# Performance work log

Hardware: AMD Instinct MI355X
Metric: run time of the kernel (lower is better)

## Reference

```python
import jax, jax.numpy as jnp
import numpy as np

N_NODES = 50000
N_EDGES = 800000
IN_DIM = 128
HID = 64
ZDIM = 64
N_GRAPHS = 64


def gcn_conv(x, W, b, src, dst, n):
    # PyG GCNConv: add self-loops, symmetric deg^-1/2 normalization,
    # linear transform then gather-scatter aggregation.
    h = x @ W  # [N, out]
    loops = jnp.arange(n, dtype=src.dtype)
    s = jnp.concatenate([src, loops])
    d = jnp.concatenate([dst, loops])
    deg = jnp.zeros((n,), h.dtype).at[d].add(1.0)  # includes self-loops -> >=1
    dinv = jax.lax.rsqrt(deg)
    norm = dinv[s] * dinv[d]  # [E+N]
    msg = h[s] * norm[:, None]  # gather [E+N, out]
    out = jnp.zeros_like(h).at[d].add(msg)  # scatter-add
    return out + b


def mean_pool(h, batch, num_graphs):
    sums = jax.ops.segment_sum(h, batch, num_segments=num_graphs)
    cnt = jax.ops.segment_sum(jnp.ones((h.shape[0],), h.dtype), batch,
                              num_segments=num_graphs)
    return sums / jnp.maximum(cnt, 1.0)[:, None]


def setup_inputs() -> dict:
    key = jax.random.key(0)
    ks = jax.random.split(key, 9)
    x = jax.random.normal(ks[0], (N_NODES, IN_DIM), jnp.float32)
    edge_index = jax.random.randint(ks[1], (2, N_EDGES), 0, N_NODES, jnp.int64 if jax.config.jax_enable_x64 else jnp.int32)
    batch = jnp.sort(jax.random.randint(ks[2], (N_NODES,), 0, N_GRAPHS))
    s1 = 1.0 / np.sqrt(IN_DIM)
    s2 = 1.0 / np.sqrt(HID)
    W1 = jax.random.uniform(ks[3], (IN_DIM, HID), jnp.float32, -s1, s1)
    b1 = jnp.zeros((HID,), jnp.float32)
    Wmu = jax.random.uniform(ks[4], (HID, ZDIM), jnp.float32, -s2, s2)
    bmu = jnp.zeros((ZDIM,), jnp.float32)
    Wsig = jax.random.uniform(ks[5], (HID, ZDIM), jnp.float32, -s2, s2)
    bsig = jnp.zeros((ZDIM,), jnp.float32)
    return {"x": x, "edge_index": edge_index, "batch": batch,
            "num_graphs": N_GRAPHS, "W1": W1, "b1": b1,
            "Wmu": Wmu, "bmu": bmu, "Wsig": Wsig, "bsig": bsig}


def reference(x, edge_index, batch, num_graphs, W1, b1, Wmu, bmu, Wsig, bsig):
    src, dst = edge_index[0], edge_index[1]
    n = x.shape[0]
    h = jax.nn.elu(gcn_conv(x, W1, b1, src, dst, n))
    z_mu = mean_pool(jax.nn.elu(gcn_conv(h, Wmu, bmu, src, dst, n)), batch, num_graphs)
    z_sigma = mean_pool(jax.nn.elu(gcn_conv(h, Wsig, bsig, src, dst, n)), batch, num_graphs)
    return (z_mu, z_sigma)
```

## Files before the change

### kernel.cpp

```cpp
#include <hip/hip_runtime.h>
#include <hip/hip_fp16.h>


#define IN_DIM 128
#define HID 64
#define ZDIM 64
#define N_GRAPHS 64
#define SCAN_B 1024

__device__ __forceinline__ float elu1(float x) {
    return x > 0.f ? x : expm1f(x);
}

#define ACC8(RV, MV) do { \
    const __half2* _hp = (const __half2*)&(RV); \
    float2 _f0 = __half22float2(_hp[0]); \
    float2 _f1 = __half22float2(_hp[1]); \
    float2 _f2 = __half22float2(_hp[2]); \
    float2 _f3 = __half22float2(_hp[3]); \
    acc[0] = fmaf((MV), _f0.x, acc[0]); \
    acc[1] = fmaf((MV), _f0.y, acc[1]); \
    acc[2] = fmaf((MV), _f1.x, acc[2]); \
    acc[3] = fmaf((MV), _f1.y, acc[3]); \
    acc[4] = fmaf((MV), _f2.x, acc[4]); \
    acc[5] = fmaf((MV), _f2.y, acc[5]); \
    acc[6] = fmaf((MV), _f3.x, acc[6]); \
    acc[7] = fmaf((MV), _f3.y, acc[7]); \
  } while (0)

__global__ void k_count(const int* __restrict__ dst, int* __restrict__ kc,
                        int* __restrict__ rank, int E) {
    int e = blockIdx.x * blockDim.x + threadIdx.x;
    if (e < E) rank[e] = atomicAdd(&kc[dst[e]], 1);
}

__global__ __launch_bounds__(SCAN_B) void k_scan1(const int* __restrict__ kc,
                                                  int* __restrict__ bsum, int n) {
    __shared__ int wpart[16];
    int tid = threadIdx.x, lane = tid & 63, w = tid >> 6;
    int i = blockIdx.x * SCAN_B + tid;
    int v = (i < n) ? kc[i] : 0;
#pragma unroll
    for (int d = 1; d < 64; d <<= 1) v += __shfl_xor(v, d, 64);
    if (lane == 0) wpart[w] = v;
    __syncthreads();
    if (tid < 16) {
        int t = wpart[tid];
#pragma unroll
        for (int d = 1; d < 16; d <<= 1) t += __shfl_xor(t, d, 64);
        if (tid == 0) bsum[blockIdx.x] = t;
    }
}

__global__ __launch_bounds__(SCAN_B) void k_scan3(const int* __restrict__ kc,
                                                  const int* __restrict__ bsum,
                                                  int* __restrict__ offs,
                                                  float* __restrict__ dinv,
                                                  int n, int nb) {
    __shared__ int wsum[16];
    __shared__ int sbase;
    int tid = threadIdx.x, lane = tid & 63, w = tid >> 6;
    if (tid < 64) {
        int v = (tid < nb) ? bsum[tid] : 0;
        int s = v;
#pragma unroll
        for (int d = 1; d < 64; d <<= 1) {
            int u = __shfl_up(s, d, 64);
            if (tid >= d) s += u;
        }
        if (tid == blockIdx.x) sbase = s - v;
    }
    int i = blockIdx.x * SCAN_B + tid;
    int v = (i < n) ? kc[i] : 0;
    int s = v;
#pragma unroll
    for (int d = 1; d < 64; d <<= 1) {
        int u = __shfl_up(s, d, 64);
        if (lane >= d) s += u;
    }
    if (lane == 63) wsum[w] = s;
    __syncthreads();
    if (tid < 16) {
        int t = wsum[tid];
#pragma unroll
        for (int d = 1; d < 16; d <<= 1) {
            int u = __shfl_up(t, d, 64);
            if (tid >= d) t += u;
        }
        wsum[tid] = t;
    }
    __syncthreads();
    int base = sbase + ((w == 0) ? 0 : wsum[w - 1]);
    if (i < n) {
        offs[i + 1] = base + s;
        dinv[i] = 1.0f / sqrtf(1.0f + (float)v);
        if (i == 0) offs[0] = 0;
    }
}

__global__ void k_fill(const int* __restrict__ src, const int* __restrict__ dst,
                       const int* __restrict__ rank, const int* __restrict__ offs,
                       int* __restrict__ csr, int E) {
    int e = blockIdx.x * blockDim.x + threadIdx.x;
    if (e < E) csr[offs[dst[e]] + rank[e]] = src[e];
}

__global__ __launch_bounds__(256) void k_mm1(const float* __restrict__ x,
                                             const float* __restrict__ W,
                                             const float* __restrict__ dinv,
                                             __half* __restrict__ ts1h, int n) {
    __shared__ float xs[64 * 68];
    __shared__ float ws[64 * 68];
    const int tid = threadIdx.x;
    const int m0 = blockIdx.x * 64;
    const int j = tid & 15;
    const int i = tid >> 4;

    const float4* x4 = (const float4*)x;
    const float4* W4 = (const float4*)W;

    float4 acc[4];
#pragma unroll
    for (int r = 0; r < 4; ++r) acc[r] = make_float4(0.f, 0.f, 0.f, 0.f);

    for (int kk = 0; kk < IN_DIM; kk += 64) {
        __syncthreads();
        for (int idx = tid; idx < 64 * 16; idx += 256) {
            int row = idx >> 4, c4 = idx & 15;
            float4 v = make_float4(0.f, 0.f, 0.f, 0.f);
            if (m0 + row < n) v = x4[(size_t)(m0 + row) * 32 + (kk >> 2) + c4];
            *(float4*)&xs[row * 68 + 4 * c4] = v;
            *(float4*)&ws[row * 68 + 4 * c4] = W4[(size_t)(kk + row) * 16 + c4];
        }
        __syncthreads();
#pragma unroll 1
        for (int k4 = 0; k4 < 16; ++k4) {
            float4 a[4];
#pragma unroll
            for (int r = 0; r < 4; ++r)
                a[r] = *(const float4*)&xs[(4 * i + r) * 68 + 4 * k4];
#pragma unroll
            for (int kc = 0; kc < 4; ++kc) {
                float4 bv = *(const float4*)&ws[(4 * k4 + kc) * 68 + 4 * j];
#pragma unroll
                for (int r = 0; r < 4; ++r) {
                    float av = (&a[r].x)[kc];
                    acc[r].x = fmaf(av, bv.x, acc[r].x);
                    acc[r].y = fmaf(av, bv.y, acc[r].y);
                    acc[r].z = fmaf(av, bv.z, acc[r].z);
                    acc[r].w = fmaf(av, bv.w, acc[r].w);
                }
            }
        }
    }

#pragma unroll
    for (int r = 0; r < 4; ++r) {
        int row = m0 + 4 * i + r;
        if (row < n) {
            float di = dinv[row];
            float4 tv = acc[r];
            __half2* p = (__half2*)&ts1h[(size_t)row * HID + 4 * j];
            p[0] = __floats2half2_rn(tv.x * di, tv.y * di);
            p[1] = __floats2half2_rn(tv.z * di, tv.w * di);
        }
    }
}

__global__ __launch_bounds__(256) void k_gather_hh(const int* __restrict__ off,
                                                   const int* __restrict__ csr,
                                                   const float* __restrict__ dinv,
                                                   const __half* __restrict__ ts,
                                                   const float* __restrict__ b1,
                                                   __half* __restrict__ hh, int n) {
    int node = blockIdx.x * 4 + (threadIdx.x >> 6);
    if (node >= n) return;
    int lane = threadIdx.x & 63;
    int g = lane >> 3, sub = lane & 7;
    int s0 = off[node], s1 = off[node + 1];
    float acc[8];
#pragma unroll
    for (int j = 0; j < 8; ++j) acc[j] = 0.f;

    if (s1 > s0) {
        int last = s1 - 1;
        int p0 = s0 + g, p1 = p0 + 8, p2 = p0 + 16, p3 = p0 + 24;
        int i0 = csr[p0 < s1 ? p0 : last];
        int i1 = csr[p1 < s1 ? p1 : last];
        int i2 = csr[p2 < s1 ? p2 : last];
        int i3 = csr[p3 < s1 ? p3 : last];
        float4 r0 = *(const float4*)&ts[(size_t)i0 * 64 + sub * 8];
        float4 r1 = *(const float4*)&ts[(size_t)i1 * 64 + sub * 8];
        float4 r2 = *(const float4*)&ts[(size_t)i2 * 64 + sub * 8];
        float4 r3 = *(const float4*)&ts[(size_t)i3 * 64 + sub * 8];
        float m0 = (p0 < s1) ? 1.f : 0.f;
        float m1 = (p1 < s1) ? 1.f : 0.f;
        float m2 = (p2 < s1) ? 1.f : 0.f;
        float m3 = (p3 < s1) ? 1.f : 0.f;
        ACC8(r0, m0);
        ACC8(r1, m1);
        ACC8(r2, m2);
        ACC8(r3, m3);
        for (int k = s0 + 32 + g; k < s1; k += 8) {
            int iv = csr[k];
            float4 rv = *(const float4*)&ts[(size_t)iv * 64 + sub * 8];
            ACC8(rv, 1.f);
        }
    }

#pragma unroll
    for (int j = 0; j < 8; ++j) {
        acc[j] += __shfl_xor(acc[j], 8, 64);
        acc[j] += __shfl_xor(acc[j], 16, 64);
        acc[j] += __shfl_xor(acc[j], 32, 64);
    }

    if (g == 0) {
        float4 sr = *(const float4*)&ts[(size_t)node * 64 + sub * 8];
        const __half2* sh = (const __half2*)&sr;
        float di = dinv[node];
        const float4* b4 = (const float4*)b1;
        float4 ba = b4[sub * 2], bb = b4[sub * 2 + 1];
        float2 f0 = __half22float2(sh[0]);
        float2 f1 = __half22float2(sh[1]);
        float2 f2 = __half22float2(sh[2]);
        float2 f3 = __half22float2(sh[3]);
        float e0 = elu1((acc[0] + f0.x) * di + ba.x) * di;
        float e1 = elu1((acc[1] + f0.y) * di + ba.y) * di;
        float e2 = elu1((acc[2] + f1.x) * di + ba.z) * di;
        float e3 = elu1((acc[3] + f1.y) * di + ba.w) * di;
        float e4 = elu1((acc[4] + f2.x) * di + bb.x) * di;
        float e5 = elu1((acc[5] + f2.y) * di + bb.y) * di;
        float e6 = elu1((acc[6] + f3.x) * di + bb.z) * di;
        float e7 = elu1((acc[7] + f3.y) * di + bb.w) * di;
        float4 outv;
        __half2* op = (__half2*)&outv;
        op[0] = __floats2half2_rn(e0, e1);
        op[1] = __floats2half2_rn(e2, e3);
        op[2] = __floats2half2_rn(e4, e5);
        op[3] = __floats2half2_rn(e6, e7);
        *(float4*)&hh[(size_t)node * 64 + sub * 8] = outv;
    }
}

__global__ __launch_bounds__(256) void k_gather_g(const int* __restrict__ off,
                                                  const int* __restrict__ csr,
                                                  const float* __restrict__ dinv,
                                                  const __half* __restrict__ hh,
                                                  float* __restrict__ gout, int n) {
    int node = blockIdx.x * 4 + (threadIdx.x >> 6);
    if (node >= n) return;
    int lane = threadIdx.x & 63;
    int g = lane >> 3, sub = lane & 7;
    int s0 = off[node], s1 = off[node + 1];
    float acc[8];
#pragma unroll
    for (int j = 0; j < 8; ++j) acc[j] = 0.f;

    if (s1 > s0) {
        int last = s1 - 1;
        int p0 = s0 + g, p1 = p0 + 8, p2 = p0 + 16, p3 = p0 + 24;
        int i0 = csr[p0 < s1 ? p0 : last];
        int i1 = csr[p1 < s1 ? p1 : last];
        int i2 = csr[p2 < s1 ? p2 : last];
        int i3 = csr[p3 < s1 ? p3 : last];
        float4 r0 = *(const float4*)&hh[(size_t)i0 * 64 + sub * 8];
        float4 r1 = *(const float4*)&hh[(size_t)i1 * 64 + sub * 8];
        float4 r2 = *(const float4*)&hh[(size_t)i2 * 64 + sub * 8];
        float4 r3 = *(const float4*)&hh[(size_t)i3 * 64 + sub * 8];
        float m0 = (p0 < s1) ? 1.f : 0.f;
        float m1 = (p1 < s1) ? 1.f : 0.f;
        float m2 = (p2 < s1) ? 1.f : 0.f;
        float m3 = (p3 < s1) ? 1.f : 0.f;
        ACC8(r0, m0);
        ACC8(r1, m1);
        ACC8(r2, m2);
        ACC8(r3, m3);
        for (int k = s0 + 32 + g; k < s1; k += 8) {
            int iv = csr[k];
            float4 rv = *(const float4*)&hh[(size_t)iv * 64 + sub * 8];
            ACC8(rv, 1.f);
        }
    }

#pragma unroll
    for (int j = 0; j < 8; ++j) {
        acc[j] += __shfl_xor(acc[j], 8, 64);
        acc[j] += __shfl_xor(acc[j], 16, 64);
        acc[j] += __shfl_xor(acc[j], 32, 64);
    }

    if (g == 0) {
        float4 sr = *(const float4*)&hh[(size_t)node * 64 + sub * 8];
        const __half2* sh = (const __half2*)&sr;
        float di = dinv[node];
        float2 f0 = __half22float2(sh[0]);
        float2 f1 = __half22float2(sh[1]);
        float2 f2 = __half22float2(sh[2]);
        float2 f3 = __half22float2(sh[3]);
        float o0 = (acc[0] + f0.x) * di;
        float o1 = (acc[1] + f0.y) * di;
        float o2 = (acc[2] + f1.x) * di;
        float o3 = (acc[3] + f1.y) * di;
        float o4 = (acc[4] + f2.x) * di;
        float o5 = (acc[5] + f2.y) * di;
        float o6 = (acc[6] + f3.x) * di;
        float o7 = (acc[7] + f3.y) * di;
        *(float4*)&gout[(size_t)node * 64 + sub * 8] = make_float4(o0, o1, o2, o3);
        *(float4*)&gout[(size_t)node * 64 + sub * 8 + 4] = make_float4(o4, o5, o6, o7);
    }
}

__global__ __launch_bounds__(256) void k_mm_pool(const float* __restrict__ g,
                                                 const float* __restrict__ Wmu,
                                                 const float* __restrict__ Wsig,
                                                 const float* __restrict__ bmu,
                                                 const float* __restrict__ bsig,
                                                 const int* __restrict__ batch,
                                                 float* __restrict__ sums, int n) {
    __shared__ float hs[64 * 68];
    __shared__ float wc[64 * 132];
    __shared__ int bs[64];
    const int tid = threadIdx.x;
    const int m0 = blockIdx.x * 64;
    const int j = tid & 15;
    const int i = tid >> 4;

    const float4* g4 = (const float4*)g;
    const float4* Wm4 = (const float4*)Wmu;
    const float4* Ws4 = (const float4*)Wsig;
    for (int idx = tid; idx < 64 * 16; idx += 256) {
        int row = idx >> 4, c4 = idx & 15;
        float4 v = make_float4(0.f, 0.f, 0.f, 0.f);
        if (m0 + row < n) v = g4[(size_t)(m0 + row) * 16 + c4];
        *(float4*)&hs[row * 68 + 4 * c4] = v;
        *(float4*)&wc[row * 132 + 4 * c4] = Wm4[(size_t)row * 16 + c4];
        *(float4*)&wc[row * 132 + 64 + 4 * c4] = Ws4[(size_t)row * 16 + c4];
    }
    if (tid < 64) bs[tid] = (m0 + tid < n) ? batch[m0 + tid] : -1;
    __syncthreads();

    float4 accm[4], accs[4];
#pragma unroll
    for (int r = 0; r < 4; ++r) {
        accm[r] = make_float4(0.f, 0.f, 0.f, 0.f);
        accs[r] = make_float4(0.f, 0.f, 0.f, 0.f);
    }

#pragma unroll 1
    for (int k4 = 0; k4 < 16; ++k4) {
        float4 a[4];
#pragma unroll
        for (int r = 0; r < 4; ++r)
            a[r] = *(const float4*)&hs[(4 * i + r) * 68 + 4 * k4];
#pragma unroll
        for (int kc = 0; kc < 4; ++kc) {
            float4 bm = *(const float4*)&wc[(4 * k4 + kc) * 132 + 4 * j];
            float4 bsv = *(const float4*)&wc[(4 * k4 + kc) * 132 + 64 + 4 * j];
#pragma unroll
            for (int r = 0; r < 4; ++r) {
                float av = (&a[r].x)[kc];
                accm[r].x = fmaf(av, bm.x, accm[r].x);
                accm[r].y = fmaf(av, bm.y, accm[r].y);
                accm[r].z = fmaf(av, bm.z, accm[r].z);
                accm[r].w = fmaf(av, bm.w, accm[r].w);
                accs[r].x = fmaf(av, bsv.x, accs[r].x);
                accs[r].y = fmaf(av, bsv.y, accs[r].y);
                accs[r].z = fmaf(av, bsv.z, accs[r].z);
                accs[r].w = fmaf(av, bsv.w, accs[r].w);
            }
        }
    }

    float4 bm = ((const float4*)bmu)[j];
    float4 bg = ((const float4*)bsig)[j];
    __syncthreads();

#pragma unroll
    for (int r = 0; r < 4; ++r) {
        int row = 4 * i + r;
        float4 m = accm[r], s = accs[r];
        m.x = elu1(m.x + bm.x);
        m.y = elu1(m.y + bm.y);
        m.z = elu1(m.z + bm.z);
        m.w = elu1(m.w + bm.w);
        s.x = elu1(s.x + bg.x);
        s.y = elu1(s.y + bg.y);
        s.z = elu1(s.z + bg.z);
        s.w = elu1(s.w + bg.w);
        *(float4*)&wc[row * 132 + 4 * j] = m;
        *(float4*)&wc[row * 132 + 64 + 4 * j] = s;
    }
    __syncthreads();

    int d = tid & 127, seg = tid >> 7;
    int base = (d < 64) ? d : (64 * 64 - 64 + d);
    float acc = 0.f;
    int gcur = -1;
    int r0 = seg * 32;
    for (int r = r0; r < r0 + 32; ++r) {
        int gb = bs[r];
        if (gb < 0) break;
        float v = wc[r * 132 + d];
        if (gb != gcur) {
            if (gcur >= 0) atomicAdd(&sums[base + gcur * 64], acc);
            acc = 0.f;
            gcur = gb;
        }
        acc += v;
    }
    if (gcur >= 0) atomicAdd(&sums[base + gcur * 64], acc);
}

__global__ void k_pool_final(const float* __restrict__ sums,
                             const int* __restrict__ batch,
                             float* __restrict__ out, int n) {
    int i = blockIdx.x * blockDim.x + threadIdx.x;
    if (i >= 2 * N_GRAPHS * ZDIM) return;
    int g = (i >> 6) & 63;
    int lo = 0, hi = n;
    while (lo < hi) { int m = (lo + hi) >> 1; if (batch[m] < g) lo = m + 1; else hi = m; }
    int s = lo;
    lo = s; hi = n;
    while (lo < hi) { int m = (lo + hi) >> 1; if (batch[m] < g + 1) lo = m + 1; else hi = m; }
    float c = fmaxf((float)(lo - s), 1.0f);
    out[i] = sums[i] / c;
}

extern "C" void kernel_launch(void* const* d_in, const int* in_sizes, int n_in,
                              void* d_out, int out_size, void* d_ws, size_t ws_size,
                              hipStream_t stream) {
    const float* x    = (const float*)d_in[0];
    const int*   ei   = (const int*)d_in[1];
    const int*   batch= (const int*)d_in[2];
    const float* W1   = (const float*)d_in[4];
    const float* b1   = (const float*)d_in[5];
    const float* Wmu  = (const float*)d_in[6];
    const float* bmu  = (const float*)d_in[7];
    const float* Wsig = (const float*)d_in[8];
    const float* bsig = (const float*)d_in[9];
    float* out = (float*)d_out;

    const int n = in_sizes[0] / IN_DIM;
    const int E = in_sizes[1] / 2;
    const int* src = ei;
    const int* dst = ei + E;
    const int NSB = (n + SCAN_B - 1) / SCAN_B;

    float* ws = (float*)d_ws;
    size_t off_w = 0;
    int*   kc   = (int*)(ws + off_w); off_w += 50048;
    float* sums = ws + off_w; off_w += 8192;
    float* dinv = ws + off_w; off_w += 50048;
    int*   offs = (int*)(ws + off_w); off_w += 50056;
    int*   bsum = (int*)(ws + off_w); off_w += 64;
    int*   rank = (int*)(ws + off_w); off_w += 800000;
    int*   csr  = (int*)(ws + off_w); off_w += 800000;
    off_w = (off_w + 15) & ~(size_t)15;
    const size_t BIG = (size_t)n * 64;
    __half* ts1h = (__half*)(ws + off_w); off_w += BIG / 2;
    __half* hh   = (__half*)(ws + off_w); off_w += BIG / 2;
    float*  gbuf = ws + off_w; off_w += BIG;

    const int gE  = (E + 255) / 256;
    const int gNW = (n + 3) / 4;
    const int NB  = (n + 63) / 64;

    hipMemsetAsync(kc, 0, (50048 + 8192) * sizeof(int), stream);
    k_count<<<gE, 256, 0, stream>>>(dst, kc, rank, E);
    k_scan1<<<NSB, SCAN_B, 0, stream>>>(kc, bsum, n);
    k_scan3<<<NSB, SCAN_B, 0, stream>>>(kc, bsum, offs, dinv, n, NSB);
    k_fill<<<gE, 256, 0, stream>>>(src, dst, rank, offs, csr, E);

    k_mm1<<<NB, 256, 0, stream>>>(x, W1, dinv, ts1h, n);
    k_gather_hh<<<gNW, 256, 0, stream>>>(offs, csr, dinv, ts1h, b1, hh, n);

    k_gather_g<<<gNW, 256, 0, stream>>>(offs, csr, dinv, hh, gbuf, n);

    k_mm_pool<<<NB, 256, 0, stream>>>(gbuf, Wmu, Wsig, bmu, bsig, batch, sums, n);
    k_pool_final<<<(2 * N_GRAPHS * ZDIM + 255) / 256, 256, 0, stream>>>(sums, batch, out, n);
}
```

Baseline: 238.1 us.

## Split fp16 feature buffers into two 32-column halves for gather kernels

The 64-wide fp16 node feature arrays are stored as two separate 32-column planar buffers, and each gather kernel launches twice as many blocks, each handling one half for four nodes. Each wavefront now gathers 16 neighbours in parallel with 64-byte rows instead of 8 with 128-byte rows, so there are more independent loads in flight per node. Blocks for the two halves are interleaved so both halves of a node group run close together in time. The cost is twice the CSR index reads, an extra shuffle-reduction step, and more blocks overall.

```diff
diff --git a/kernel.cpp b/kernel.cpp
--- a/kernel.cpp
+++ b/kernel.cpp
@@ -108,7 +108,8 @@
 __global__ __launch_bounds__(256) void k_mm1(const float* __restrict__ x,
                                              const float* __restrict__ W,
                                              const float* __restrict__ dinv,
-                                             __half* __restrict__ ts1h, int n) {
+                                             __half* __restrict__ tsA,
+                                             __half* __restrict__ tsB, int n) {
     __shared__ float xs[64 * 68];
     __shared__ float ws[64 * 68];
     const int tid = threadIdx.x;
@@ -160,9 +161,13 @@
         if (row < n) {
             float di = dinv[row];
             float4 tv = acc[r];
-            __half2* p = (__half2*)&ts1h[(size_t)row * HID + 4 * j];
-            p[0] = __floats2half2_rn(tv.x * di, tv.y * di);
-            p[1] = __floats2half2_rn(tv.z * di, tv.w * di);
+            __half2 h0 = __floats2half2_rn(tv.x * di, tv.y * di);
+            __half2 h1 = __floats2half2_rn(tv.z * di, tv.w * di);
+            __half2* p = (j < 8)
+                ? (__half2*)&tsA[(size_t)row * 32 + 4 * j]
+                : (__half2*)&tsB[(size_t)row * 32 + 4 * (j - 8)];
+            p[0] = h0;
+            p[1] = h1;
         }
     }
 }
@@ -170,57 +175,58 @@
 __global__ __launch_bounds__(256) void k_gather_hh(const int* __restrict__ off,
                                                    const int* __restrict__ csr,
                                                    const float* __restrict__ dinv,
-                                                   const __half* __restrict__ ts,
+                                                   const __half* __restrict__ tsA,
+                                                   const __half* __restrict__ tsB,
                                                    const float* __restrict__ b1,
-                                                   __half* __restrict__ hh, int n) {
-    int node = blockIdx.x * 4 + (threadIdx.x >> 6);
+                                                   __half* __restrict__ hhA,
+                                                   __half* __restrict__ hhB, int n) {
+    int bid = blockIdx.x;
+    int half = (bid >> 2) & 1;
+    int jb = (bid >> 3) * 4 + (bid & 3);
+    int node = jb * 4 + (threadIdx.x >> 6);
     if (node >= n) return;
+    const __half* T = half ? tsB : tsA;
+    __half* H = half ? hhB : hhA;
     int lane = threadIdx.x & 63;
-    int g = lane >> 3, sub = lane & 7;
+    int g = lane >> 2, sub = lane & 3;
     int s0 = off[node], s1 = off[node + 1];
     float acc[8];
 #pragma unroll
-    for (int j = 0; j < 8; ++j) acc[j] = 0.f;
+    for (int q = 0; q < 8; ++q) acc[q] = 0.f;
 
     if (s1 > s0) {
         int last = s1 - 1;
-        int p0 = s0 + g, p1 = p0 + 8, p2 = p0 + 16, p3 = p0 + 24;
+        int p0 = s0 + g, p1 = p0 + 16;
         int i0 = csr[p0 < s1 ? p0 : last];
         int i1 = csr[p1 < s1 ? p1 : last];
-        int i2 = csr[p2 < s1 ? p2 : last];
-        int i3 = csr[p3 < s1 ? p3 : last];
-        float4 r0 = *(const float4*)&ts[(size_t)i0 * 64 + sub * 8];
-        float4 r1 = *(const float4*)&ts[(size_t)i1 * 64 + sub * 8];
-        float4 r2 = *(const float4*)&ts[(size_t)i2 * 64 + sub * 8];
-        float4 r3 = *(const float4*)&ts[(size_t)i3 * 64 + sub * 8];
+        float4 r0 = *(const float4*)&T[(size_t)i0 * 32 + sub * 8];
+        float4 r1 = *(const float4*)&T[(size_t)i1 * 32 + sub * 8];
         float m0 = (p0 < s1) ? 1.f : 0.f;
         float m1 = (p1 < s1) ? 1.f : 0.f;
-        float m2 = (p2 < s1) ? 1.f : 0.f;
-        float m3 = (p3 < s1) ? 1.f : 0.f;
         ACC8(r0, m0);
         ACC8(r1, m1);
-        ACC8(r2, m2);
-        ACC8(r3, m3);
-        for (int k = s0 + 32 + g; k < s1; k += 8) {
+        for (int k = s0 + 32 + g; k < s1; k += 16) {
             int iv = csr[k];
-            float4 rv = *(const float4*)&ts[(size_t)iv * 64 + sub * 8];
+            float4 rv = *(const float4*)&T[(size_t)iv * 32 + sub * 8];
             ACC8(rv, 1.f);
         }
     }
 
 #pragma unroll
-    for (int j = 0; j < 8; ++j) {
-        acc[j] += __shfl_xor(acc[j], 8, 64);
-        acc[j] += __shfl_xor(acc[j], 16, 64);
-        acc[j] += __shfl_xor(acc[j], 32, 64);
+    for (int q = 0; q < 8; ++q) {
+        acc[q] += __shfl_xor(acc[q], 4, 64);
+        acc[q] += __shfl_xor(acc[q], 8, 64);
+        acc[q] += __shfl_xor(acc[q], 16, 64);
+        acc[q] += __shfl_xor(acc[q], 32, 64);
     }
 
     if (g == 0) {
-        float4 sr = *(const float4*)&ts[(size_t)node * 64 + sub * 8];
+        float4 sr = *(const float4*)&T[(size_t)node * 32 + sub * 8];
         const __half2* sh = (const __half2*)&sr;
         float di = dinv[node];
         const float4* b4 = (const float4*)b1;
-        float4 ba = b4[sub * 2], bb = b4[sub * 2 + 1];
+        float4 ba = b4[half * 8 + sub * 2];
+        float4 bb = b4[half * 8 + sub * 2 + 1];
         float2 f0 = __half22float2(sh[0]);
         float2 f1 = __half22float2(sh[1]);
         float2 f2 = __half22float2(sh[2]);
@@ -239,59 +245,57 @@
         op[1] = __floats2half2_rn(e2, e3);
         op[2] = __floats2half2_rn(e4, e5);
         op[3] = __floats2half2_rn(e6, e7);
-        *(float4*)&hh[(size_t)node * 64 + sub * 8] = outv;
+        *(float4*)&H[(size_t)node * 32 + sub * 8] = outv;
     }
 }
 
 __global__ __launch_bounds__(256) void k_gather_g(const int* __restrict__ off,
                                                   const int* __restrict__ csr,
                                                   const float* __restrict__ dinv,
-                                                  const __half* __restrict__ hh,
+                                                  const __half* __restrict__ hhA,
+                                                  const __half* __restrict__ hhB,
                                                   float* __restrict__ gout, int n) {
-    int node = blockIdx.x * 4 + (threadIdx.x >> 6);
+    int bid = blockIdx.x;
+    int half = (bid >> 2) & 1;
+    int jb = (bid >> 3) * 4 + (bid & 3);
+    int node = jb * 4 + (threadIdx.x >> 6);
     if (node >= n) return;
+    const __half* T = half ? hhB : hhA;
     int lane = threadIdx.x & 63;
-    int g = lane >> 3, sub = lane & 7;
+    int g = lane >> 2, sub = lane & 3;
     int s0 = off[node], s1 = off[node + 1];
     float acc[8];
 #pragma unroll
-    for (int j = 0; j < 8; ++j) acc[j] = 0.f;
+    for (int q = 0; q < 8; ++q) acc[q] = 0.f;
 
     if (s1 > s0) {
         int last = s1 - 1;
-        int p0 = s0 + g, p1 = p0 + 8, p2 = p0 + 16, p3 = p0 + 24;
+        int p0 = s0 + g, p1 = p0 + 16;
         int i0 = csr[p0 < s1 ? p0 : last];
         int i1 = csr[p1 < s1 ? p1 : last];
-        int i2 = csr[p2 < s1 ? p2 : last];
-        int i3 = csr[p3 < s1 ? p3 : last];
-        float4 r0 = *(const float4*)&hh[(size_t)i0 * 64 + sub * 8];
-        float4 r1 = *(const float4*)&hh[(size_t)i1 * 64 + sub * 8];
-        float4 r2 = *(const float4*)&hh[(size_t)i2 * 64 + sub * 8];
-        float4 r3 = *(const float4*)&hh[(size_t)i3 * 64 + sub * 8];
+        float4 r0 = *(const float4*)&T[(size_t)i0 * 32 + sub * 8];
+        float4 r1 = *(const float4*)&T[(size_t)i1 * 32 + sub * 8];
         float m0 = (p0 < s1) ? 1.f : 0.f;
         float m1 = (p1 < s1) ? 1.f : 0.f;
-        float m2 = (p2 < s1) ? 1.f : 0.f;
-        float m3 = (p3 < s1) ? 1.f : 0.f;
         ACC8(r0, m0);
         ACC8(r1, m1);
-        ACC8(r2, m2);
-        ACC8(r3, m3);
-        for (int k = s0 + 32 + g; k < s1; k += 8) {
+        for (int k = s0 + 32 + g; k < s1; k += 16) {
             int iv = csr[k];
-            float4 rv = *(const float4*)&hh[(size_t)iv * 64 + sub * 8];
+            float4 rv = *(const float4*)&T[(size_t)iv * 32 + sub * 8];
             ACC8(rv, 1.f);
         }
     }
 
 #pragma unroll
-    for (int j = 0; j < 8; ++j) {
-        acc[j] += __shfl_xor(acc[j], 8, 64);
-        acc[j] += __shfl_xor(acc[j], 16, 64);
-        acc[j] += __shfl_xor(acc[j], 32, 64);
+    for (int q = 0; q < 8; ++q) {
+        acc[q] += __shfl_xor(acc[q], 4, 64);
+        acc[q] += __shfl_xor(acc[q], 8, 64);
+        acc[q] += __shfl_xor(acc[q], 16, 64);
+        acc[q] += __shfl_xor(acc[q], 32, 64);
     }
 
     if (g == 0) {
-        float4 sr = *(const float4*)&hh[(size_t)node * 64 + sub * 8];
+        float4 sr = *(const float4*)&T[(size_t)node * 32 + sub * 8];
         const __half2* sh = (const __half2*)&sr;
         float di = dinv[node];
         float2 f0 = __half22float2(sh[0]);
@@ -306,8 +310,9 @@
         float o5 = (acc[5] + f2.y) * di;
         float o6 = (acc[6] + f3.x) * di;
         float o7 = (acc[7] + f3.y) * di;
-        *(float4*)&gout[(size_t)node * 64 + sub * 8] = make_float4(o0, o1, o2, o3);
-        *(float4*)&gout[(size_t)node * 64 + sub * 8 + 4] = make_float4(o4, o5, o6, o7);
+        float* gp = &gout[(size_t)node * 64 + half * 32 + sub * 8];
+        *(float4*)gp = make_float4(o0, o1, o2, o3);
+        *(float4*)(gp + 4) = make_float4(o4, o5, o6, o7);
     }
 }
 
@@ -457,14 +462,18 @@
     int*   rank = (int*)(ws + off_w); off_w += 800000;
     int*   csr  = (int*)(ws + off_w); off_w += 800000;
     off_w = (off_w + 15) & ~(size_t)15;
-    const size_t BIG = (size_t)n * 64;
-    __half* ts1h = (__half*)(ws + off_w); off_w += BIG / 2;
-    __half* hh   = (__half*)(ws + off_w); off_w += BIG / 2;
-    float*  gbuf = ws + off_w; off_w += BIG;
+    const size_t HALF16 = (size_t)50048 * 16;
+    __half* tsA = (__half*)(ws + off_w); off_w += HALF16;
+    __half* tsB = (__half*)(ws + off_w); off_w += HALF16;
+    __half* hhA = (__half*)(ws + off_w); off_w += HALF16;
+    __half* hhB = (__half*)(ws + off_w); off_w += HALF16;
+    float*  gbuf = ws + off_w; off_w += (size_t)50048 * 64;
 
     const int gE  = (E + 255) / 256;
-    const int gNW = (n + 3) / 4;
     const int NB  = (n + 63) / 64;
+    const int bph = (n + 3) / 4;
+    const int bph4 = (bph + 3) & ~3;
+    const int gG = 2 * bph4;
 
     hipMemsetAsync(kc, 0, (50048 + 8192) * sizeof(int), stream);
     k_count<<<gE, 256, 0, stream>>>(dst, kc, rank, E);
@@ -472,10 +481,10 @@
     k_scan3<<<NSB, SCAN_B, 0, stream>>>(kc, bsum, offs, dinv, n, NSB);
     k_fill<<<gE, 256, 0, stream>>>(src, dst, rank, offs, csr, E);
 
-    k_mm1<<<NB, 256, 0, stream>>>(x, W1, dinv, ts1h, n);
-    k_gather_hh<<<gNW, 256, 0, stream>>>(offs, csr, dinv, ts1h, b1, hh, n);
-
-    k_gather_g<<<gNW, 256, 0, stream>>>(offs, csr, dinv, hh, gbuf, n);
+    k_mm1<<<NB, 256, 0, stream>>>(x, W1, dinv, tsA, tsB, n);
+    k_gather_hh<<<gG, 256, 0, stream>>>(offs, csr, dinv, tsA, tsB, b1, hhA, hhB, n);
+
+    k_gather_g<<<gG, 256, 0, stream>>>(offs, csr, dinv, hhA, hhB, gbuf, n);
 
     k_mm_pool<<<NB, 256, 0, stream>>>(gbuf, Wmu, Wsig, bmu, bsig, batch, sums, n);
     k_pool_final<<<(2 * N_GRAPHS * ZDIM + 255) / 256, 256, 0, stream>>>(sums, batch, out, n);
```

Result: slower. 272.7 us (+14.5%).

## Use MFMA fp16 matrix cores for the two dense transforms

Applied to the files above, without the earlier changes.

Replaces the shared-memory FP32 FMA tiles in k_mm1 and k_mm_pool with fp16 MFMA 16x16x32 instructions. A new kernel pre-packs W1, Wmu and Wsig into per-lane fragment layout. The x and g inputs are read straight from global memory and converted to fp16 in registers. This cuts ALU time and shared-memory staging, at the cost of fp16 rounding of the inputs and weights and one extra small kernel launch.

```diff
diff --git a/kernel.cpp b/kernel.cpp
--- a/kernel.cpp
+++ b/kernel.cpp
@@ -7,6 +7,9 @@
 #define ZDIM 64
 #define N_GRAPHS 64
 #define SCAN_B 1024
+
+typedef _Float16 half8 __attribute__((ext_vector_type(8)));
+typedef float f32x4 __attribute__((ext_vector_type(4)));
 
 __device__ __forceinline__ float elu1(float x) {
     return x > 0.f ? x : expm1f(x);
@@ -105,64 +108,70 @@
     if (e < E) csr[offs[dst[e]] + rank[e]] = src[e];
 }
 
+__global__ void k_wfrag(const float* __restrict__ W1,
+                        const float* __restrict__ Wmu,
+                        const float* __restrict__ Wsig,
+                        __half* __restrict__ F1,
+                        __half* __restrict__ Fmu,
+                        __half* __restrict__ Fsig) {
+    int e = blockIdx.x * 256 + threadIdx.x;
+    if (e < 8192) {
+        int j = e & 7, l = (e >> 3) & 63, ct = (e >> 9) & 3, ks = e >> 11;
+        F1[e] = __float2half(W1[(ks * 32 + ((l >> 4) & 3) * 8 + j) * 64 + ct * 16 + (l & 15)]);
+    }
+    if (e < 4096) {
+        int j = e & 7, l = (e >> 3) & 63, ct = (e >> 9) & 3, ks = e >> 11;
+        int widx = (ks * 32 + ((l >> 4) & 3) * 8 + j) * 64 + ct * 16 + (l & 15);
+        Fmu[e] = __float2half(Wmu[widx]);
+        Fsig[e] = __float2half(Wsig[widx]);
+    }
+}
+
 __global__ __launch_bounds__(256) void k_mm1(const float* __restrict__ x,
-                                             const float* __restrict__ W,
+                                             const __half* __restrict__ F1,
                                              const float* __restrict__ dinv,
                                              __half* __restrict__ ts1h, int n) {
-    __shared__ float xs[64 * 68];
-    __shared__ float ws[64 * 68];
-    const int tid = threadIdx.x;
-    const int m0 = blockIdx.x * 64;
-    const int j = tid & 15;
-    const int i = tid >> 4;
-
-    const float4* x4 = (const float4*)x;
-    const float4* W4 = (const float4*)W;
-
-    float4 acc[4];
-#pragma unroll
-    for (int r = 0; r < 4; ++r) acc[r] = make_float4(0.f, 0.f, 0.f, 0.f);
-
-    for (int kk = 0; kk < IN_DIM; kk += 64) {
-        __syncthreads();
-        for (int idx = tid; idx < 64 * 16; idx += 256) {
-            int row = idx >> 4, c4 = idx & 15;
-            float4 v = make_float4(0.f, 0.f, 0.f, 0.f);
-            if (m0 + row < n) v = x4[(size_t)(m0 + row) * 32 + (kk >> 2) + c4];
-            *(float4*)&xs[row * 68 + 4 * c4] = v;
-            *(float4*)&ws[row * 68 + 4 * c4] = W4[(size_t)(kk + row) * 16 + c4];
-        }
-        __syncthreads();
-#pragma unroll 1
-        for (int k4 = 0; k4 < 16; ++k4) {
-            float4 a[4];
-#pragma unroll
-            for (int r = 0; r < 4; ++r)
-                a[r] = *(const float4*)&xs[(4 * i + r) * 68 + 4 * k4];
-#pragma unroll
-            for (int kc = 0; kc < 4; ++kc) {
-                float4 bv = *(const float4*)&ws[(4 * k4 + kc) * 68 + 4 * j];
-#pragma unroll
-                for (int r = 0; r < 4; ++r) {
-                    float av = (&a[r].x)[kc];
-                    acc[r].x = fmaf(av, bv.x, acc[r].x);
-                    acc[r].y = fmaf(av, bv.y, acc[r].y);
-                    acc[r].z = fmaf(av, bv.z, acc[r].z);
-                    acc[r].w = fmaf(av, bv.w, acc[r].w);
-                }
-            }
-        }
-    }
-
+    int l = threadIdx.x & 63;
+    int wave = threadIdx.x >> 6;
+    int m0 = blockIdx.x * 64 + wave * 16;
+    int row_a = m0 + (l & 15);
+    if (row_a >= n) row_a = n - 1;
+    int kg = l >> 4;
+
+    f32x4 acc0 = {0.f, 0.f, 0.f, 0.f};
+    f32x4 acc1 = acc0, acc2 = acc0, acc3 = acc0;
+
+    const float* xr = x + (size_t)row_a * IN_DIM + kg * 8;
+#pragma unroll
+    for (int ks = 0; ks < 4; ++ks) {
+        float4 xa = *(const float4*)(xr + ks * 32);
+        float4 xb = *(const float4*)(xr + ks * 32 + 4);
+        half8 a;
+        a[0] = (_Float16)xa.x; a[1] = (_Float16)xa.y;
+        a[2] = (_Float16)xa.z; a[3] = (_Float16)xa.w;
+        a[4] = (_Float16)xb.x; a[5] = (_Float16)xb.y;
+        a[6] = (_Float16)xb.z; a[7] = (_Float16)xb.w;
+        const __half* fb = F1 + ((size_t)(ks * 4) * 64 + l) * 8;
+        half8 b0 = *(const half8*)(fb);
+        half8 b1 = *(const half8*)(fb + 512);
+        half8 b2 = *(const half8*)(fb + 1024);
+        half8 b3 = *(const half8*)(fb + 1536);
+        acc0 = __builtin_amdgcn_mfma_f32_16x16x32_f16(a, b0, acc0, 0, 0, 0);
+        acc1 = __builtin_amdgcn_mfma_f32_16x16x32_f16(a, b1, acc1, 0, 0, 0);
+        acc2 = __builtin_amdgcn_mfma_f32_16x16x32_f16(a, b2, acc2, 0, 0, 0);
+        acc3 = __builtin_amdgcn_mfma_f32_16x16x32_f16(a, b3, acc3, 0, 0, 0);
+    }
+    int col = l & 15;
 #pragma unroll
     for (int r = 0; r < 4; ++r) {
-        int row = m0 + 4 * i + r;
+        int row = m0 + kg * 4 + r;
         if (row < n) {
             float di = dinv[row];
-            float4 tv = acc[r];
-            __half2* p = (__half2*)&ts1h[(size_t)row * HID + 4 * j];
-            p[0] = __floats2half2_rn(tv.x * di, tv.y * di);
-            p[1] = __floats2half2_rn(tv.z * di, tv.w * di);
+            __half* p = &ts1h[(size_t)row * 64 + col];
+            p[0]  = __float2half(acc0[r] * di);
+            p[16] = __float2half(acc1[r] * di);
+            p[32] = __float2half(acc2[r] * di);
+            p[48] = __float2half(acc3[r] * di);
         }
     }
 }
@@ -312,84 +321,62 @@
 }
 
 __global__ __launch_bounds__(256) void k_mm_pool(const float* __restrict__ g,
-                                                 const float* __restrict__ Wmu,
-                                                 const float* __restrict__ Wsig,
+                                                 const __half* __restrict__ Fmu,
+                                                 const __half* __restrict__ Fsig,
                                                  const float* __restrict__ bmu,
                                                  const float* __restrict__ bsig,
                                                  const int* __restrict__ batch,
                                                  float* __restrict__ sums, int n) {
-    __shared__ float hs[64 * 68];
     __shared__ float wc[64 * 132];
     __shared__ int bs[64];
     const int tid = threadIdx.x;
-    const int m0 = blockIdx.x * 64;
-    const int j = tid & 15;
-    const int i = tid >> 4;
-
-    const float4* g4 = (const float4*)g;
-    const float4* Wm4 = (const float4*)Wmu;
-    const float4* Ws4 = (const float4*)Wsig;
-    for (int idx = tid; idx < 64 * 16; idx += 256) {
-        int row = idx >> 4, c4 = idx & 15;
-        float4 v = make_float4(0.f, 0.f, 0.f, 0.f);
-        if (m0 + row < n) v = g4[(size_t)(m0 + row) * 16 + c4];
-        *(float4*)&hs[row * 68 + 4 * c4] = v;
-        *(float4*)&wc[row * 132 + 4 * c4] = Wm4[(size_t)row * 16 + c4];
-        *(float4*)&wc[row * 132 + 64 + 4 * c4] = Ws4[(size_t)row * 16 + c4];
-    }
+    int l = tid & 63, wave = tid >> 6;
+    int m0 = blockIdx.x * 64;
+    int row_a = m0 + wave * 16 + (l & 15);
+    if (row_a >= n) row_a = n - 1;
+    int kg = l >> 4;
+
+    f32x4 am[4], as[4];
+#pragma unroll
+    for (int ct = 0; ct < 4; ++ct) {
+        am[ct] = (f32x4){0.f, 0.f, 0.f, 0.f};
+        as[ct] = (f32x4){0.f, 0.f, 0.f, 0.f};
+    }
+
+    const float* gr = g + (size_t)row_a * 64 + kg * 8;
+#pragma unroll
+    for (int ks = 0; ks < 2; ++ks) {
+        float4 xa = *(const float4*)(gr + ks * 32);
+        float4 xb = *(const float4*)(gr + ks * 32 + 4);
+        half8 a;
+        a[0] = (_Float16)xa.x; a[1] = (_Float16)xa.y;
+        a[2] = (_Float16)xa.z; a[3] = (_Float16)xa.w;
+        a[4] = (_Float16)xb.x; a[5] = (_Float16)xb.y;
+        a[6] = (_Float16)xb.z; a[7] = (_Float16)xb.w;
+        const __half* fm = Fmu + ((size_t)(ks * 4) * 64 + l) * 8;
+        const __half* fs = Fsig + ((size_t)(ks * 4) * 64 + l) * 8;
+#pragma unroll
+        for (int ct = 0; ct < 4; ++ct) {
+            half8 bm = *(const half8*)(fm + ct * 512);
+            half8 bv = *(const half8*)(fs + ct * 512);
+            am[ct] = __builtin_amdgcn_mfma_f32_16x16x32_f16(a, bm, am[ct], 0, 0, 0);
+            as[ct] = __builtin_amdgcn_mfma_f32_16x16x32_f16(a, bv, as[ct], 0, 0, 0);
+        }
+    }
+
     if (tid < 64) bs[tid] = (m0 + tid < n) ? batch[m0 + tid] : -1;
-    __syncthreads();
-
-    float4 accm[4], accs[4];
-#pragma unroll
-    for (int r = 0; r < 4; ++r) {
-        accm[r] = make_float4(0.f, 0.f, 0.f, 0.f);
-        accs[r] = make_float4(0.f, 0.f, 0.f, 0.f);
-    }
-
-#pragma unroll 1
-    for (int k4 = 0; k4 < 16; ++k4) {
-        float4 a[4];
-#pragma unroll
-        for (int r = 0; r < 4; ++r)
-            a[r] = *(const float4*)&hs[(4 * i + r) * 68 + 4 * k4];
-#pragma unroll
-        for (int kc = 0; kc < 4; ++kc) {
-            float4 bm = *(const float4*)&wc[(4 * k4 + kc) * 132 + 4 * j];
-            float4 bsv = *(const float4*)&wc[(4 * k4 + kc) * 132 + 64 + 4 * j];
-#pragma unroll
-            for (int r = 0; r < 4; ++r) {
-                float av = (&a[r].x)[kc];
-                accm[r].x = fmaf(av, bm.x, accm[r].x);
-                accm[r].y = fmaf(av, bm.y, accm[r].y);
-                accm[r].z = fmaf(av, bm.z, accm[r].z);
-                accm[r].w = fmaf(av, bm.w, accm[r].w);
-                accs[r].x = fmaf(av, bsv.x, accs[r].x);
-                accs[r].y = fmaf(av, bsv.y, accs[r].y);
-                accs[r].z = fmaf(av, bsv.z, accs[r].z);
-                accs[r].w = fmaf(av, bsv.w, accs[r].w);
-            }
-        }
-    }
-
-    float4 bm = ((const float4*)bmu)[j];
-    float4 bg = ((const float4*)bsig)[j];
-    __syncthreads();
-
-#pragma unroll
-    for (int r = 0; r < 4; ++r) {
-        int row = 4 * i + r;
-        float4 m = accm[r], s = accs[r];
-        m.x = elu1(m.x + bm.x);
-        m.y = elu1(m.y + bm.y);
-        m.z = elu1(m.z + bm.z);
-        m.w = elu1(m.w + bm.w);
-        s.x = elu1(s.x + bg.x);
-        s.y = elu1(s.y + bg.y);
-        s.z = elu1(s.z + bg.z);
-        s.w = elu1(s.w + bg.w);
-        *(float4*)&wc[row * 132 + 4 * j] = m;
-        *(float4*)&wc[row * 132 + 64 + 4 * j] = s;
+
+    int col = l & 15;
+#pragma unroll
+    for (int ct = 0; ct < 4; ++ct) {
+        float bM = bmu[ct * 16 + col];
+        float bS = bsig[ct * 16 + col];
+#pragma unroll
+        for (int r = 0; r < 4; ++r) {
+            int rr = wave * 16 + kg * 4 + r;
+            wc[rr * 132 + ct * 16 + col] = elu1(am[ct][r] + bM);
+            wc[rr * 132 + 64 + ct * 16 + col] = elu1(as[ct][r] + bS);
+        }
     }
     __syncthreads();
 
@@ -457,6 +444,9 @@
     int*   rank = (int*)(ws + off_w); off_w += 800000;
     int*   csr  = (int*)(ws + off_w); off_w += 800000;
     off_w = (off_w + 15) & ~(size_t)15;
+    __half* F1   = (__half*)(ws + off_w); off_w += 4096;
+    __half* Fmu  = (__half*)(ws + off_w); off_w += 2048;
+    __half* Fsig = (__half*)(ws + off_w); off_w += 2048;
     const size_t BIG = (size_t)n * 64;
     __half* ts1h = (__half*)(ws + off_w); off_w += BIG / 2;
     __half* hh   = (__half*)(ws + off_w); off_w += BIG / 2;
@@ -467,16 +457,17 @@
     const int NB  = (n + 63) / 64;
 
     hipMemsetAsync(kc, 0, (50048 + 8192) * sizeof(int), stream);
+    k_wfrag<<<32, 256, 0, stream>>>(W1, Wmu, Wsig, F1, Fmu, Fsig);
     k_count<<<gE, 256, 0, stream>>>(dst, kc, rank, E);
     k_scan1<<<NSB, SCAN_B, 0, stream>>>(kc, bsum, n);
     k_scan3<<<NSB, SCAN_B, 0, stream>>>(kc, bsum, offs, dinv, n, NSB);
     k_fill<<<gE, 256, 0, stream>>>(src, dst, rank, offs, csr, E);
 
-    k_mm1<<<NB, 256, 0, stream>>>(x, W1, dinv, ts1h, n);
+    k_mm1<<<NB, 256, 0, stream>>>(x, F1, dinv, ts1h, n);
     k_gather_hh<<<gNW, 256, 0, stream>>>(offs, csr, dinv, ts1h, b1, hh, n);
 
     k_gather_g<<<gNW, 256, 0, stream>>>(offs, csr, dinv, hh, gbuf, n);
 
-    k_mm_pool<<<NB, 256, 0, stream>>>(gbuf, Wmu, Wsig, bmu, bsig, batch, sums, n);
+    k_mm_pool<<<NB, 256, 0, stream>>>(gbuf, Fmu, Fsig, bmu, bsig, batch, sums, n);
     k_pool_final<<<(2 * N_GRAPHS * ZDIM + 255) / 256, 256, 0, stream>>>(sums, batch, out, n);
 }
```

After: 220.2 us. 7.5% less time.
